# Performance work log

Measured on AMD Instinct MI355X. Metric: run time of the kernel, lower is better.

The kernel has to match this reference:

```python
import jax, jax.numpy as jnp
import numpy as np
import math

D_MODEL = 1024
N_HEADS = 16
DH = D_MODEL // N_HEADS
THETA = 10000.0


def _rope_tables(S):
    # freqs: (dh/2,)
    inv_freq = 1.0 / (THETA ** (jnp.arange(0, DH, 2, dtype=jnp.float32) / DH))
    ang = jnp.arange(S, dtype=jnp.float32)[:, None] * inv_freq[None, :]  # (S, dh/2)
    cos = jnp.concatenate([jnp.cos(ang), jnp.cos(ang)], axis=-1)  # (S, dh)
    sin = jnp.concatenate([jnp.sin(ang), jnp.sin(ang)], axis=-1)
    return cos, sin


def _apply_rope(x, cos, sin):
    # x: (B, S, H, dh); rotate-half RoPE
    x1, x2 = jnp.split(x, 2, axis=-1)
    rot = jnp.concatenate([-x2, x1], axis=-1)
    c = cos[None, :, None, :]
    s = sin[None, :, None, :]
    return x * c + rot * s


def setup_inputs() -> dict:
    key = jax.random.key(0)
    k1, k2, k3 = jax.random.split(key, 3)
    x = jax.random.normal(k1, (4, 2048, D_MODEL), dtype=jnp.float32)
    qkv = 0.01 * jax.random.normal(k2, (3 * D_MODEL, D_MODEL), dtype=jnp.float32)
    wo = 0.01 * jax.random.normal(k3, (D_MODEL, D_MODEL), dtype=jnp.float32)
    return {"x": x, "qkv": qkv, "wo": wo}


def reference(x, qkv, wo):
    B, S, D = x.shape
    QKV = x @ qkv.T  # (B, S, 3D)
    Q, K, V = jnp.split(QKV, 3, axis=-1)
    q = Q.reshape(B, S, N_HEADS, DH)
    k = K.reshape(B, S, N_HEADS, DH)
    v = V.reshape(B, S, N_HEADS, DH)
    cos, sin = _rope_tables(S)
    q = _apply_rope(q, cos, sin)
    k = _apply_rope(k, cos, sin)
    # (B, H, S, dh)
    q = q.transpose(0, 2, 1, 3)
    k = k.transpose(0, 2, 1, 3)
    v = v.transpose(0, 2, 1, 3)
    scores = jnp.einsum("bhsd,bhtd->bhst", q, k) / math.sqrt(float(DH))
    mask = jnp.tril(jnp.ones((S, S), dtype=scores.dtype))
    scores = scores * mask
    # faithful to original: any exact-zero entry (masked or incidental) -> -inf
    scores = jnp.where(scores == 0.0, -jnp.inf, scores)
    attn = jax.nn.softmax(scores, axis=-1)
    out = jnp.einsum("bhst,bhtd->bhsd", attn, v)  # (B, H, S, dh)
    out = out.transpose(0, 2, 1, 3).reshape(B, S, D)
    return out @ wo.T
```

## Files before the change

### kernel.cpp

```cpp
#include <hip/hip_runtime.h>
#include <math.h>

typedef __bf16 bf16x8 __attribute__((ext_vector_type(8)));
typedef __bf16 bf16x4 __attribute__((ext_vector_type(4)));
typedef float  floatx4 __attribute__((ext_vector_type(4)));
typedef float  floatx2 __attribute__((ext_vector_type(2)));

#define AS1(p) ((__attribute__((address_space(1))) void*)(p))
#define AS3(p) ((__attribute__((address_space(3))) void*)(p))

#define MASKV (-1.0e30f)
#define SOFTMAX_SCALE_LOG2 0.1803368801111244f
#define ROPE_LOG2F 0.4152410118609203f

#define BARRIER do { __builtin_amdgcn_sched_barrier(0); \
                     __builtin_amdgcn_s_barrier(); \
                     __builtin_amdgcn_sched_barrier(0); } while (0)

__global__ __launch_bounds__(256)
void cvt3_kernel(const float* __restrict__ x, const float* __restrict__ qkv,
                 const float* __restrict__ wo, __bf16* __restrict__ xb,
                 __bf16* __restrict__ qkvb, __bf16* __restrict__ wob,
                 float* __restrict__ rt)
{
    const int bi = blockIdx.x;
    if (bi >= 12288) {
        const int e0 = (bi - 12288) * 1024 + threadIdx.x * 4;
#pragma unroll
        for (int j = 0; j < 4; ++j) {
            const int e = e0 + j;
            const int s = e >> 5, d = e & 31;
            const float f = exp2f(-(float)d * ROPE_LOG2F);
            float sn, cs;
            sincosf((float)s * f, &sn, &cs);
            floatx2 t; t[0] = cs; t[1] = sn;
            *(floatx2*)(rt + e * 2) = t;
        }
        return;
    }
    const float* src;
    __bf16* dst;
    int base;
    if (bi < 8192)       { src = x;   dst = xb;   base = bi * 1024; }
    else if (bi < 11264) { src = qkv; dst = qkvb; base = (bi - 8192) * 1024; }
    else                 { src = wo;  dst = wob;  base = (bi - 11264) * 1024; }

    const int i = base + threadIdx.x * 4;
    const floatx4 v = *(const floatx4*)(src + i);
    bf16x4 o;
    o[0] = (__bf16)v[0]; o[1] = (__bf16)v[1];
    o[2] = (__bf16)v[2]; o[3] = (__bf16)v[3];
    *(bf16x4*)(dst + i) = o;
}

__device__ __forceinline__ void gemm_pipe(const __bf16* __restrict__ Ap,
                                          const __bf16* __restrict__ Bp,
                                          const int m0, const int n0,
                                          __bf16* smem, floatx4 (&acc)[4][4])
{
    const int tid  = threadIdx.x;
    const int wave = tid >> 6;
    const int lane = tid & 63;
    const int quad = lane >> 4;
    const int l16  = lane & 15;
    const int wr   = wave >> 2;
    const int wc   = wave & 3;

    const int arow = wr * 32 + l16;
    const int brow = (wc & 1) * 64 + l16;
    const int bsel = (wc >> 1) * 8192;
    const int swz  = (l16 & 7) << 4;
    int coff[2];
    coff[0] = (( (quad << 4))        ^ swz) >> 1;
    coff[1] = ((64 | (quad << 4))    ^ swz) >> 1;

    auto stageA = [&](int buf, int h, int k0) {
        const int o = tid << 4;
        const int r = o >> 7;
        const int c = (o & 127) ^ ((r & 7) << 4);
        const __bf16* src = Ap + (size_t)(m0 + h * 64 + r) * 1024 + k0 + (c >> 1);
        __builtin_amdgcn_global_load_lds(AS1(src),
            AS3(smem + buf * 24576 + h * 4096 + wave * 512), 16, 0, 0);
    };
    auto stageB = [&](int buf, int h, int k0) {
#pragma unroll
        for (int q = 0; q < 2; ++q) {
            const int o = (q * 512 + tid) << 4;
            const int r = o >> 7;
            const int c = (o & 127) ^ ((r & 7) << 4);
            const __bf16* src = Bp + (size_t)(n0 + h * 128 + r) * 1024 + k0 + (c >> 1);
            __builtin_amdgcn_global_load_lds(AS1(src),
                AS3(smem + buf * 24576 + 8192 + h * 8192 + (q * 8 + wave) * 512), 16, 0, 0);
        }
    };

#define RDA(P, qm, fm, ks) (*(const bf16x8*)(smem + (P) * 24576 + (qm) * 4096 \
                             + ((arow + (fm) * 16) << 6) + coff[ks]))
#define RDB(P, g, ks)      (*(const bf16x8*)(smem + (P) * 24576 + 8192 + bsel \
                             + ((brow + (g) * 16) << 6) + coff[ks]))
#define MFMA8(MB, NB, AV, BV) do { \
    _Pragma("unroll") for (int fm_ = 0; fm_ < 2; ++fm_) \
    _Pragma("unroll") for (int gi_ = 0; gi_ < 2; ++gi_) \
    _Pragma("unroll") for (int ks_ = 0; ks_ < 2; ++ks_) \
        acc[(MB) + fm_][(NB) + gi_] = __builtin_amdgcn_mfma_f32_16x16x32_bf16( \
            AV[fm_][ks_], BV[gi_][ks_], acc[(MB) + fm_][(NB) + gi_], 0, 0, 0); \
} while (0)

    stageA(0, 0, 0);  stageB(0, 0, 0);  stageA(0, 1, 0);  stageB(0, 1, 0);
    stageA(1, 0, 64); stageB(1, 0, 64); stageA(1, 1, 64);
    asm volatile("s_waitcnt vmcnt(4)" ::: "memory");
    BARRIER;

    bf16x8 a0[2][2], a1[2][2], b0[2][2], b1[2][2];

#define TILE(JT, P) do { \
    const int kn_ = ((JT) + 2) * 64; \
    _Pragma("unroll") for (int f_ = 0; f_ < 2; ++f_) \
    _Pragma("unroll") for (int k_ = 0; k_ < 2; ++k_) a0[f_][k_] = RDA(P, 0, f_, k_); \
    _Pragma("unroll") for (int g_ = 0; g_ < 2; ++g_) \
    _Pragma("unroll") for (int k_ = 0; k_ < 2; ++k_) b0[g_][k_] = RDB(P, g_, k_); \
    if ((JT) + 1 < 16) stageB(1 - (P), 1, ((JT) + 1) * 64); \
    BARRIER; \
    __builtin_amdgcn_s_setprio(1); MFMA8(0, 0, a0, b0); __builtin_amdgcn_s_setprio(0); \
    BARRIER; \
    _Pragma("unroll") for (int g_ = 0; g_ < 2; ++g_) \
    _Pragma("unroll") for (int k_ = 0; k_ < 2; ++k_) b1[g_][k_] = RDB(P, 2 + g_, k_); \
    if ((JT) + 2 < 16) stageA(P, 0, kn_); \
    BARRIER; \
    __builtin_amdgcn_s_setprio(1); MFMA8(0, 2, a0, b1); __builtin_amdgcn_s_setprio(0); \
    BARRIER; \
    _Pragma("unroll") for (int f_ = 0; f_ < 2; ++f_) \
    _Pragma("unroll") for (int k_ = 0; k_ < 2; ++k_) a1[f_][k_] = RDA(P, 1, f_, k_); \
    if ((JT) + 2 < 16) stageB(P, 0, kn_); \
    BARRIER; \
    __builtin_amdgcn_s_setprio(1); MFMA8(2, 2, a1, b1); __builtin_amdgcn_s_setprio(0); \
    BARRIER; \
    if ((JT) + 2 < 16) stageA(P, 1, kn_); \
    BARRIER; \
    __builtin_amdgcn_s_setprio(1); MFMA8(2, 0, a1, b0); __builtin_amdgcn_s_setprio(0); \
    if ((JT) + 2 < 16)      { asm volatile("s_waitcnt vmcnt(4)" ::: "memory"); } \
    else if ((JT) + 1 < 16) { asm volatile("s_waitcnt vmcnt(0)" ::: "memory"); } \
    BARRIER; \
} while (0)

    for (int it = 0; it < 8; ++it) {
        TILE(2 * it, 0);
        TILE(2 * it + 1, 1);
    }
#undef TILE
#undef RDA
#undef RDB
#undef MFMA8
}

__global__ __launch_bounds__(512, 2)
void gemm_rope_kernel(const __bf16* __restrict__ A, const __bf16* __restrict__ BT,
                      __bf16* __restrict__ Qr, __bf16* __restrict__ Kr,
                      __bf16* __restrict__ Vt, const float* __restrict__ rt)
{
    extern __shared__ __align__(16) __bf16 smem[];
    const int id  = blockIdx.x;
    const int xcd = id & 7, lid = id >> 3;
    const int tm  = xcd * 8 + lid / 12;
    const int tn  = lid % 12;
    const int m0  = tm * 128, n0 = tn * 256;

    floatx4 acc[4][4] = {};
    gemm_pipe(A, BT, m0, n0, smem, acc);

    const int tid  = threadIdx.x;
    const int wave = tid >> 6;
    const int lane = tid & 63;
    const int quad = lane >> 4, l16 = lane & 15;
    const int wr   = wave >> 2, wc = wave & 3;

    const int gn0    = n0 + wc * 64;
    const int region = gn0 >> 10;
    const int h      = (gn0 >> 6) & 15;

    if (region == 2) {
#pragma unroll
        for (int f = 0; f < 4; ++f) {
            const int gm = m0 + (f >> 1) * 64 + wr * 32 + (f & 1) * 16 + quad * 4;
            const int b = gm >> 11, s = gm & 2047;
#pragma unroll
            for (int g = 0; g < 4; ++g) {
                const int d = g * 16 + l16;
                bf16x4 w;
#pragma unroll
                for (int r = 0; r < 4; ++r) w[r] = (__bf16)acc[f][g][r];
                *(bf16x4*)(Vt + ((size_t)(b * 16 + h) * 64 + d) * 2048 + s) = w;
            }
        }
    } else {
        __bf16* dst = region ? Kr : Qr;
        const float sc = region ? 1.0f : SOFTMAX_SCALE_LOG2;
#pragma unroll
        for (int g = 0; g < 2; ++g) {
            const int d1 = g * 16 + l16;
#pragma unroll
            for (int f = 0; f < 4; ++f) {
                const int gm0 = m0 + (f >> 1) * 64 + wr * 32 + (f & 1) * 16 + quad * 4;
                const int b = gm0 >> 11, s0 = gm0 & 2047;
#pragma unroll
                for (int r = 0; r < 4; ++r) {
                    const floatx2 t = *(const floatx2*)(rt + ((s0 + r) * 32 + d1) * 2);
                    const float a1 = acc[f][g][r];
                    const float a2 = acc[f][g + 2][r];
                    __bf16* row = dst + ((size_t)((b * 16 + h) * 2048 + s0 + r)) * 64;
                    row[d1]      = (__bf16)((a1 * t[0] - a2 * t[1]) * sc);
                    row[d1 + 32] = (__bf16)((a2 * t[0] + a1 * t[1]) * sc);
                }
            }
        }
    }
}

__global__ __launch_bounds__(512, 2)
void gemm_bt_kernel(const __bf16* __restrict__ A, const __bf16* __restrict__ BT,
                    float* __restrict__ C)
{
    extern __shared__ __align__(16) __bf16 smem[];
    const int id  = blockIdx.x;
    const int xcd = id & 7, lid = id >> 3;
    const int tm  = xcd * 8 + (lid >> 2);
    const int tn  = lid & 3;
    const int m0  = tm * 128, n0 = tn * 256;

    floatx4 acc[4][4] = {};
    gemm_pipe(A, BT, m0, n0, smem, acc);

    const int tid  = threadIdx.x;
    const int wave = tid >> 6, lane = tid & 63;
    const int quad = lane >> 4, l16 = lane & 15;
    const int wr   = wave >> 2, wc = wave & 3;

#pragma unroll
    for (int f = 0; f < 4; ++f) {
        const int row = m0 + (f >> 1) * 64 + wr * 32 + (f & 1) * 16 + quad * 4;
#pragma unroll
        for (int g = 0; g < 4; ++g) {
            const int col = n0 + wc * 64 + g * 16 + l16;
#pragma unroll
            for (int r = 0; r < 4; ++r)
                C[(size_t)(row + r) * 1024 + col] = acc[f][g][r];
        }
    }
}

__global__ __launch_bounds__(256, 4)
void attn_kernel(const __bf16* __restrict__ Qr, const __bf16* __restrict__ Kr,
                 const __bf16* __restrict__ Vt, __bf16* __restrict__ ctx)
{
    __shared__ __align__(16) __bf16 Ks[64 * 64];
    __shared__ __align__(16) __bf16 Vs[64 * 64];
    __shared__ __align__(16) __bf16 plds[4][16 * 72];

    const int bh   = blockIdx.x;
    const int b    = bh >> 4, h = bh & 15;
    const int tid  = threadIdx.x;
    const int wave = tid >> 6;
    const int lane = tid & 63;
    const int quad = lane >> 4, l16 = lane & 15;
    const int sw   = l16 & 7;

    const __bf16* Qb = Qr + (size_t)bh * 2048 * 64;
    const __bf16* Kb = Kr + (size_t)bh * 2048 * 64;
    const __bf16* Vb = Vt + (size_t)bh * 64 * 2048;
    __bf16* Pw = &plds[wave][0];

    const int row0 = tid >> 3, jg0 = (tid & 7) ^ (row0 & 7);
    const int c1   = 256 + tid;
    const int row1 = c1 >> 3, jg1 = (c1 & 7) ^ (row1 & 7);

    const __bf16* pK0 = Kb + (size_t)row0 * 64 + jg0 * 8;
    const __bf16* pK1 = Kb + (size_t)row1 * 64 + jg1 * 8;
    const __bf16* pV0 = Vb + (size_t)row0 * 2048 + jg0 * 8;
    const __bf16* pV1 = Vb + (size_t)row1 * 2048 + jg1 * 8;

    const int tiles[2] = { (int)blockIdx.y, 31 - (int)blockIdx.y };

    for (int pass = 0; pass < 2; ++pass) {
        const int tq    = tiles[pass];
        const int q0    = tq * 64 + wave * 16;
        const int qa    = q0 + l16;
        const int ntile = tq + 1;

        bf16x8 bq[2];
#pragma unroll
        for (int t = 0; t < 2; ++t)
            bq[t] = *(const bf16x8*)(Qb + (q0 + l16) * 64 + t * 32 + quad * 8);

        floatx4 o[4] = {};
        float lpart = 0.f;

        bf16x8 rk0 = *(const bf16x8*)pK0;
        bf16x8 rk1 = *(const bf16x8*)pK1;
        bf16x8 rv0 = *(const bf16x8*)pV0;
        bf16x8 rv1 = *(const bf16x8*)pV1;

        __syncthreads();

        for (int t = 0; t < ntile; ++t) {
            asm volatile("s_waitcnt vmcnt(0)" ::: "memory");
            *(bf16x8*)(Ks + tid * 8)        = rk0;
            *(bf16x8*)(Ks + 2048 + tid * 8) = rk1;
            *(bf16x8*)(Vs + tid * 8)        = rv0;
            *(bf16x8*)(Vs + 2048 + tid * 8) = rv1;
            asm volatile("s_waitcnt lgkmcnt(0)" ::: "memory");
            BARRIER;

            if (t + 1 < ntile) {
                rk0 = *(const bf16x8*)(pK0 + (size_t)(t + 1) * 4096);
                rk1 = *(const bf16x8*)(pK1 + (size_t)(t + 1) * 4096);
                rv0 = *(const bf16x8*)(pV0 + (t + 1) * 64);
                rv1 = *(const bf16x8*)(pV1 + (t + 1) * 64);
            }

            const int  kt     = t * 64;
            const bool masked = (t == ntile - 1);

            floatx4 s[4] = {};
            __builtin_amdgcn_s_setprio(1);
#pragma unroll
            for (int st = 0; st < 4; ++st) {
                bf16x8 ka0 = *(const bf16x8*)(Ks + (st * 16 + l16) * 64 + ((0 + quad) ^ sw) * 8);
                bf16x8 ka1 = *(const bf16x8*)(Ks + (st * 16 + l16) * 64 + ((4 + quad) ^ sw) * 8);
                s[st] = __builtin_amdgcn_mfma_f32_16x16x32_bf16(ka0, bq[0], s[st], 0, 0, 0);
                s[st] = __builtin_amdgcn_mfma_f32_16x16x32_bf16(ka1, bq[1], s[st], 0, 0, 0);
            }
            __builtin_amdgcn_s_setprio(0);

#pragma unroll
            for (int st = 0; st < 4; ++st) {
                bf16x4 w;
#pragma unroll
                for (int r = 0; r < 4; ++r) {
                    float v = s[st][r];
                    if (masked) {
                        const int key = kt + st * 16 + quad * 4 + r;
                        v = (key > qa) ? MASKV : v;
                    }
                    const float p = __builtin_amdgcn_exp2f(v);
                    lpart += p;
                    w[r] = (__bf16)p;
                }
                *(bf16x4*)(Pw + l16 * 72 + st * 16 + quad * 4) = w;
            }

            asm volatile("s_waitcnt lgkmcnt(0)" ::: "memory");
            bf16x8 ap0 = *(const bf16x8*)(Pw + l16 * 72 + quad * 8);
            bf16x8 ap1 = *(const bf16x8*)(Pw + l16 * 72 + 32 + quad * 8);

            __builtin_amdgcn_s_setprio(1);
#pragma unroll
            for (int nt = 0; nt < 4; ++nt) {
                bf16x8 bv0 = *(const bf16x8*)(Vs + (nt * 16 + l16) * 64 + ((0 + quad) ^ sw) * 8);
                bf16x8 bv1 = *(const bf16x8*)(Vs + (nt * 16 + l16) * 64 + ((4 + quad) ^ sw) * 8);
                o[nt] = __builtin_amdgcn_mfma_f32_16x16x32_bf16(ap0, bv0, o[nt], 0, 0, 0);
                o[nt] = __builtin_amdgcn_mfma_f32_16x16x32_bf16(ap1, bv1, o[nt], 0, 0, 0);
            }
            __builtin_amdgcn_s_setprio(0);

            BARRIER;
        }

        float l = lpart;
        l += __shfl_xor(l, 16, 64);
        l += __shfl_xor(l, 32, 64);
        float lr[4];
#pragma unroll
        for (int r = 0; r < 4; ++r)
            lr[r] = __shfl(l, quad * 4 + r, 64);
#pragma unroll
        for (int nt = 0; nt < 4; ++nt)
#pragma unroll
            for (int r = 0; r < 4; ++r) {
                const int srow = q0 + quad * 4 + r;
                const float inv_l = 1.0f / fmaxf(lr[r], 1e-20f);
                ctx[((size_t)(b * 2048 + srow)) * 1024 + h * 64 + nt * 16 + l16] =
                    (__bf16)(o[nt][r] * inv_l);
            }
    }
}

extern "C" void kernel_launch(void* const* d_in, const int* in_sizes, int n_in,
                              void* d_out, int out_size, void* d_ws, size_t ws_size,
                              hipStream_t stream)
{
    const float* x   = (const float*)d_in[0];
    const float* qkv = (const float*)d_in[1];
    const float* wo  = (const float*)d_in[2];
    float* out = (float*)d_out;

    char* ws = (char*)d_ws;
    const size_t MB = 1024 * 1024;
    __bf16* xb   = (__bf16*)(ws);
    __bf16* qkvb = (__bf16*)(ws + 16 * MB);
    __bf16* wob  = (__bf16*)(ws + 22 * MB);
    __bf16* Qr   = (__bf16*)(ws + 24 * MB);
    __bf16* Kr   = (__bf16*)(ws + 40 * MB);
    __bf16* Vt   = (__bf16*)(ws + 56 * MB);
    __bf16* ctx  = (__bf16*)(ws + 72 * MB);
    float*  rt   = (float*) (ws + 88 * MB);

    hipFuncSetAttribute((const void*)gemm_rope_kernel,
                        hipFuncAttributeMaxDynamicSharedMemorySize, 98304);
    hipFuncSetAttribute((const void*)gemm_bt_kernel,
                        hipFuncAttributeMaxDynamicSharedMemorySize, 98304);

    cvt3_kernel<<<12352, 256, 0, stream>>>(x, qkv, wo, xb, qkvb, wob, rt);
    gemm_rope_kernel<<<768, 512, 98304, stream>>>(xb, qkvb, Qr, Kr, Vt, rt);
    attn_kernel<<<dim3(64, 16), 256, 0, stream>>>(Qr, Kr, Vt, ctx);
    gemm_bt_kernel<<<256, 512, 98304, stream>>>(ctx, wob, out);
}
```

Baseline: 237.7 us.

## Restructure GEMM main loop into two half-tile phases with full B fragment reuse

Reorganizes the bf16 GEMM pipeline from four quarter-tile MFMA phases into two phases. Each phase loads the whole B fragment set (4 groups) into registers and reuses it across both A halves. Global-to-LDS staging is regrouped and the vmcnt waits are adjusted to match. The aim is fewer barriers and LDS reads per k-step. In exchange it holds more B registers live, which could raise VGPR pressure at 2 blocks per CU, and it changes how loads overlap with MFMAs.

Result: faster. 225.2 us (-5.3%).

```diff
diff --git a/kernel.cpp b/kernel.cpp
--- a/kernel.cpp
+++ b/kernel.cpp
@@ -98,59 +98,51 @@
                              + ((arow + (fm) * 16) << 6) + coff[ks]))
 #define RDB(P, g, ks)      (*(const bf16x8*)(smem + (P) * 24576 + 8192 + bsel \
                              + ((brow + (g) * 16) << 6) + coff[ks]))
-#define MFMA8(MB, NB, AV, BV) do { \
+#define MFMA16(MB, AH) do { \
     _Pragma("unroll") for (int fm_ = 0; fm_ < 2; ++fm_) \
-    _Pragma("unroll") for (int gi_ = 0; gi_ < 2; ++gi_) \
+    _Pragma("unroll") for (int g_ = 0; g_ < 4; ++g_) \
     _Pragma("unroll") for (int ks_ = 0; ks_ < 2; ++ks_) \
-        acc[(MB) + fm_][(NB) + gi_] = __builtin_amdgcn_mfma_f32_16x16x32_bf16( \
-            AV[fm_][ks_], BV[gi_][ks_], acc[(MB) + fm_][(NB) + gi_], 0, 0, 0); \
+        acc[(MB) + fm_][g_] = __builtin_amdgcn_mfma_f32_16x16x32_bf16( \
+            AH[fm_][ks_], b[g_][ks_], acc[(MB) + fm_][g_], 0, 0, 0); \
 } while (0)
 
-    stageA(0, 0, 0);  stageB(0, 0, 0);  stageA(0, 1, 0);  stageB(0, 1, 0);
-    stageA(1, 0, 64); stageB(1, 0, 64); stageA(1, 1, 64);
-    asm volatile("s_waitcnt vmcnt(4)" ::: "memory");
+    stageA(0, 0, 0);  stageA(0, 1, 0);  stageB(0, 0, 0);  stageB(0, 1, 0);
+    stageA(1, 0, 64); stageB(1, 0, 64); stageB(1, 1, 64);
+    asm volatile("s_waitcnt vmcnt(5)" ::: "memory");
     BARRIER;
 
-    bf16x8 a0[2][2], a1[2][2], b0[2][2], b1[2][2];
-
-#define TILE(JT, P) do { \
+    bf16x8 a[2][2], b[4][2];
+
+#define TILE2(JT, P) do { \
     const int kn_ = ((JT) + 2) * 64; \
-    _Pragma("unroll") for (int f_ = 0; f_ < 2; ++f_) \
-    _Pragma("unroll") for (int k_ = 0; k_ < 2; ++k_) a0[f_][k_] = RDA(P, 0, f_, k_); \
-    _Pragma("unroll") for (int g_ = 0; g_ < 2; ++g_) \
-    _Pragma("unroll") for (int k_ = 0; k_ < 2; ++k_) b0[g_][k_] = RDB(P, g_, k_); \
-    if ((JT) + 1 < 16) stageB(1 - (P), 1, ((JT) + 1) * 64); \
+     \
+    if ((JT) + 1 < 16) stageA(1 - (P), 1, ((JT) + 1) * 64); \
+    _Pragma("unroll") for (int fm_ = 0; fm_ < 2; ++fm_) \
+    _Pragma("unroll") for (int ks_ = 0; ks_ < 2; ++ks_) a[fm_][ks_] = RDA(P, 0, fm_, ks_); \
+    _Pragma("unroll") for (int g_ = 0; g_ < 4; ++g_) \
+    _Pragma("unroll") for (int ks_ = 0; ks_ < 2; ++ks_) b[g_][ks_] = RDB(P, g_, ks_); \
     BARRIER; \
-    __builtin_amdgcn_s_setprio(1); MFMA8(0, 0, a0, b0); __builtin_amdgcn_s_setprio(0); \
+    __builtin_amdgcn_s_setprio(1); MFMA16(0, a); __builtin_amdgcn_s_setprio(0); \
     BARRIER; \
-    _Pragma("unroll") for (int g_ = 0; g_ < 2; ++g_) \
-    _Pragma("unroll") for (int k_ = 0; k_ < 2; ++k_) b1[g_][k_] = RDB(P, 2 + g_, k_); \
-    if ((JT) + 2 < 16) stageA(P, 0, kn_); \
+     \
+    if ((JT) + 2 < 16) { stageA(P, 0, kn_); stageB(P, 0, kn_); stageB(P, 1, kn_); } \
+    _Pragma("unroll") for (int fm_ = 0; fm_ < 2; ++fm_) \
+    _Pragma("unroll") for (int ks_ = 0; ks_ < 2; ++ks_) a[fm_][ks_] = RDA(P, 1, fm_, ks_); \
     BARRIER; \
-    __builtin_amdgcn_s_setprio(1); MFMA8(0, 2, a0, b1); __builtin_amdgcn_s_setprio(0); \
-    BARRIER; \
-    _Pragma("unroll") for (int f_ = 0; f_ < 2; ++f_) \
-    _Pragma("unroll") for (int k_ = 0; k_ < 2; ++k_) a1[f_][k_] = RDA(P, 1, f_, k_); \
-    if ((JT) + 2 < 16) stageB(P, 0, kn_); \
-    BARRIER; \
-    __builtin_amdgcn_s_setprio(1); MFMA8(2, 2, a1, b1); __builtin_amdgcn_s_setprio(0); \
-    BARRIER; \
-    if ((JT) + 2 < 16) stageA(P, 1, kn_); \
-    BARRIER; \
-    __builtin_amdgcn_s_setprio(1); MFMA8(2, 0, a1, b0); __builtin_amdgcn_s_setprio(0); \
-    if ((JT) + 2 < 16)      { asm volatile("s_waitcnt vmcnt(4)" ::: "memory"); } \
+    __builtin_amdgcn_s_setprio(1); MFMA16(2, a); __builtin_amdgcn_s_setprio(0); \
+    if ((JT) + 2 < 16)      { asm volatile("s_waitcnt vmcnt(5)" ::: "memory"); } \
     else if ((JT) + 1 < 16) { asm volatile("s_waitcnt vmcnt(0)" ::: "memory"); } \
     BARRIER; \
 } while (0)
 
     for (int it = 0; it < 8; ++it) {
-        TILE(2 * it, 0);
-        TILE(2 * it + 1, 1);
+        TILE2(2 * it, 0);
+        TILE2(2 * it + 1, 1);
     }
-#undef TILE
+#undef TILE2
 #undef RDA
 #undef RDB
-#undef MFMA8
+#undef MFMA16
 }
 
 __global__ __launch_bounds__(512, 2)
```
